# Kernel tuning notes

Measured on AMD Instinct MI355X. Metric: run time of the kernel, lower is better.

## Reference

```python
import jax, jax.numpy as jnp
import numpy as np

NUM_K_HEADS = 16
NUM_V_HEADS = 32
DK = 128
DV = 128
KCONV = 4
EPS = 1e-6
KEY_DIM = NUM_K_HEADS * DK      # 2048
VALUE_DIM = NUM_V_HEADS * DV    # 4096
HIDDEN = 2048
T_TOKENS = 4096


def setup_inputs() -> dict:
    key = jax.random.key(0)
    ks = jax.random.split(key, 10)
    s = 0.02
    return {
        "hidden_states": jax.random.normal(ks[0], (T_TOKENS, HIDDEN), jnp.float32),
        "W_qkv": jax.random.normal(ks[1], (2 * KEY_DIM + VALUE_DIM, HIDDEN), jnp.float32) * s,
        "W_z": jax.random.normal(ks[2], (VALUE_DIM, HIDDEN), jnp.float32) * s,
        "W_b": jax.random.normal(ks[3], (NUM_V_HEADS, HIDDEN), jnp.float32) * s,
        "W_a": jax.random.normal(ks[4], (NUM_V_HEADS, HIDDEN), jnp.float32) * s,
        "conv_weight": jax.random.normal(ks[5], (2 * KEY_DIM + VALUE_DIM, KCONV), jnp.float32) * 0.2,
        "dt_bias": jnp.ones((NUM_V_HEADS,), jnp.float32),
        "A_log": jax.random.normal(ks[6], (NUM_V_HEADS,), jnp.float32) * 0.5,
        "norm_weight": jnp.ones((DV,), jnp.float32),
        "W_out": jax.random.normal(ks[7], (HIDDEN, VALUE_DIM), jnp.float32) * s,
    }


def _l2norm(x):
    return x * jax.lax.rsqrt(jnp.sum(x * x, axis=-1, keepdims=True) + 1e-6)


def _gdn_forward(hidden_states, W_qkv, W_z, W_b, W_a, conv_weight,
                 dt_bias, A_log, norm_weight, W_out):
    T = hidden_states.shape[0]
    # input projections
    mixed_qkv = hidden_states @ W_qkv.T                         # [T, 2K+V]
    z = (hidden_states @ W_z.T).reshape(T, NUM_V_HEADS, DV)     # gate
    b = hidden_states @ W_b.T                                   # [T, Hv]
    a = hidden_states @ W_a.T                                   # [T, Hv]

    # depthwise causal conv1d (kernel 4) + silu, no bias
    xp = jnp.pad(mixed_qkv, ((KCONV - 1, 0), (0, 0)))
    conv = sum(xp[i:i + T] * conv_weight[:, i] for i in range(KCONV))
    x = jax.nn.silu(conv)

    q = x[:, :KEY_DIM].reshape(T, NUM_K_HEADS, DK)
    k = x[:, KEY_DIM:2 * KEY_DIM].reshape(T, NUM_K_HEADS, DK)
    v = x[:, 2 * KEY_DIM:].reshape(T, NUM_V_HEADS, DV)

    rep = NUM_V_HEADS // NUM_K_HEADS  # grouped value attention: repeat q/k heads
    q = jnp.repeat(_l2norm(q), rep, axis=1)  # [T, Hv, DK]
    k = jnp.repeat(_l2norm(k), rep, axis=1)

    beta = jax.nn.sigmoid(b)                                   # [T, Hv]
    g = -jnp.exp(A_log) * jax.nn.softplus(a + dt_bias)         # [T, Hv] log-decay
    scale = DK ** -0.5

    def step(S, inp):
        qt, kt, vt, bt, gt = inp
        S = S * jnp.exp(gt)[:, None, None]                     # gated decay
        kv = jnp.einsum('hk,hkv->hv', kt, S)                   # memory readout
        delta = (vt - kv) * bt[:, None]                        # delta rule update
        S = S + jnp.einsum('hk,hv->hkv', kt, delta)
        ot = jnp.einsum('hk,hkv->hv', qt, S) * scale
        return S, ot

    S0 = jnp.zeros((NUM_V_HEADS, DK, DV), mixed_qkv.dtype)
    _, o = jax.lax.scan(step, S0, (q, k, v, beta, g))          # o: [T, Hv, DV]

    # gated RMSNorm (norm before gate)
    var = jnp.mean(o * o, axis=-1, keepdims=True)
    on = o * jax.lax.rsqrt(var + EPS) * norm_weight
    y = on * jax.nn.silu(z)

    return y.reshape(T, VALUE_DIM) @ W_out.T                   # [T, HIDDEN]


def reference(hidden_states, W_qkv, W_z, W_b, W_a, conv_weight,
              dt_bias, A_log, norm_weight, W_out):
    return _gdn_forward(hidden_states, W_qkv, W_z, W_b, W_a, conv_weight,
                        dt_bias, A_log, norm_weight, W_out)
```

## Files before the change

### kernel.cpp

```cpp
#include <hip/hip_runtime.h>
#include <cstdint>
#include <cstddef>

typedef __bf16 bf16_t;
typedef __bf16 bf16x8 __attribute__((ext_vector_type(8)));
typedef __bf16 bf16x4 __attribute__((ext_vector_type(4)));
typedef float floatx4 __attribute__((ext_vector_type(4)));

__device__ __forceinline__ void async16(const bf16_t* g, bf16_t* l) {
  __builtin_amdgcn_global_load_lds(
      (const __attribute__((address_space(1))) unsigned int*)g,
      (__attribute__((address_space(3))) unsigned int*)l, 16, 0, 0);
}

__device__ __forceinline__ void barrier_lds() {
  asm volatile("s_waitcnt lgkmcnt(0)\n\ts_barrier" ::: "memory");
}

__device__ __forceinline__ float siluf(float x) { return x / (1.f + __expf(-x)); }

#define MFMA16(a, b, c) __builtin_amdgcn_mfma_f32_16x16x32_bf16(a, b, c, 0, 0, 0)
#define WAITV(n) asm volatile("s_waitcnt vmcnt(" #n ")" ::: "memory")

__global__ __launch_bounds__(256) void k_cvt(const float* __restrict__ in,
                                             bf16_t* __restrict__ out, int n4) {
  int i = blockIdx.x * 256 + threadIdx.x;
  if (i >= n4) return;
  const float4 f = ((const float4*)in)[i];
  bf16x4 r;
  r[0] = (bf16_t)f.x; r[1] = (bf16_t)f.y; r[2] = (bf16_t)f.z; r[3] = (bf16_t)f.w;
  ((bf16x4*)out)[i] = r;
}

__global__ __launch_bounds__(256) void k_build_wba(const float* __restrict__ wb,
                                                   const float* __restrict__ wa,
                                                   bf16_t* __restrict__ out) {
  int i = blockIdx.x * 256 + threadIdx.x;
  int e = i * 4;
  int row = e >> 11;
  int col = e & 2047;
  float4 f = make_float4(0.f, 0.f, 0.f, 0.f);
  if (row < 32)      f = *(const float4*)&wb[row * 2048 + col];
  else if (row < 64) f = *(const float4*)&wa[(row - 32) * 2048 + col];
  bf16x4 r;
  r[0] = (bf16_t)f.x; r[1] = (bf16_t)f.y; r[2] = (bf16_t)f.z; r[3] = (bf16_t)f.w;
  *(bf16x4*)&out[e] = r;
}

template<bool OUT_BF16>
__global__ __launch_bounds__(256) void gemm_bt(const bf16_t* __restrict__ A,
                                               const bf16_t* __restrict__ B,
                                               void* __restrict__ Cout,
                                               int M, int N, int K) {
  __shared__ __align__(16) bf16_t As[4096];
  __shared__ __align__(16) bf16_t Bs[4096];
  const int tid  = threadIdx.x;
  const int lane = tid & 63;
  const int wave = tid >> 6;
  const int quad = lane >> 4;
  const int l16  = lane & 15;
  const int wr   = (wave >> 1) * 64;
  const int wc   = (wave & 1) * 64;
  const int m0   = blockIdx.y * 128;
  const int n0   = blockIdx.x * 128;
  const int ra   = tid >> 2;
  const int ca   = (tid & 3) * 8;

  const bf16_t* gA = A + (size_t)(m0 + ra) * K + ca;
  const bf16_t* gB = B + (size_t)(n0 + ra) * K + ca;
  bf16_t* lA = &As[tid * 8];
  bf16_t* lB = &Bs[tid * 8];

  floatx4 acc[4][4] = {};

  for (int k0 = 0; k0 < K; k0 += 32) {
    __syncthreads();
    async16(gA + k0, lA);
    async16(gA + k0 + (size_t)64 * K, lA + 2048);
    async16(gB + k0, lB);
    async16(gB + k0 + (size_t)64 * K, lB + 2048);
    __syncthreads();
    bf16x8 af[4], bfr[4];
#pragma unroll
    for (int i = 0; i < 4; ++i) {
      af[i]  = *(const bf16x8*)&As[(wr + i * 16 + l16) * 32 + quad * 8];
      bfr[i] = *(const bf16x8*)&Bs[(wc + i * 16 + l16) * 32 + quad * 8];
    }
#pragma unroll
    for (int mi = 0; mi < 4; ++mi)
#pragma unroll
      for (int ni = 0; ni < 4; ++ni)
        acc[mi][ni] = MFMA16(af[mi], bfr[ni], acc[mi][ni]);
  }

#pragma unroll
  for (int mi = 0; mi < 4; ++mi) {
#pragma unroll
    for (int ni = 0; ni < 4; ++ni) {
      const int row = m0 + wr + mi * 16 + quad * 4;
      const int col = n0 + wc + ni * 16 + l16;
#pragma unroll
      for (int r = 0; r < 4; ++r) {
        if (OUT_BF16)
          ((bf16_t*)Cout)[(size_t)(row + r) * N + col] = (bf16_t)acc[mi][ni][r];
        else
          ((float*)Cout)[(size_t)(row + r) * N + col] = acc[mi][ni][r];
      }
    }
  }
}

template<int MH, bool OUT_BF16>
__global__ __launch_bounds__(512, 1) void gemm_big(const bf16_t* __restrict__ A,
                                                   const bf16_t* __restrict__ B,
                                                   void* __restrict__ Cout,
                                                   int M, int N, int K) {
  extern __shared__ __align__(16) bf16_t sm[];
  constexpr int BM    = MH * 128;
  constexpr int MFRAG = MH * 4;
  constexpr int HF    = MFRAG / 2;
  constexpr int BUFE  = MH * 4096 + 8192;
  const int tid  = threadIdx.x;
  const int lane = tid & 63;
  const int wave = tid >> 6;
  const int quad = lane >> 4;
  const int l16  = lane & 15;
  const int wm   = wave >> 2;
  const int wn   = wave & 3;

  const int gx  = (int)gridDim.x;
  const int nwg = gx * (int)gridDim.y;
  const int id  = (int)blockIdx.y * gx + (int)blockIdx.x;
  const int cpx = nwg >> 3;
  const int sw  = (id & 7) * cpx + (id >> 3);
  const int m0  = (sw / gx) * BM;
  const int n0  = (sw % gx) * 256;

  const int lr    = lane >> 2;
  const int lslot = (lane & 3) ^ ((lane >> 3) & 3);
  const bf16_t* gA = A + (size_t)(m0 + wave * (MH * 16) + lr) * K + lslot * 8;
  const bf16_t* gB = B + (size_t)(n0 + wave * 32 + lr) * K + lslot * 8;
  const int ldsA0 = wave * (MH * 512) + lane * 8;
  const int ldsB0 = MH * 4096 + wave * 1024 + lane * 8;

#define STG_A(u, kt) {                                          \
    bf16_t* la = sm + (u) * BUFE + ldsA0;                       \
    const bf16_t* ga = gA + (size_t)(kt) * 32;                  \
    async16(ga, la);                                            \
    if constexpr (MH == 2) async16(ga + (size_t)16 * K, la + 512); }
#define STG_B(u, kt) {                                          \
    bf16_t* lb = sm + (u) * BUFE + ldsB0;                       \
    const bf16_t* gb = gB + (size_t)(kt) * 32;                  \
    async16(gb, lb);                                            \
    async16(gb + (size_t)16 * K, lb + 512); }

  int offA[MFRAG], offB[4];
#pragma unroll
  for (int i = 0; i < MFRAG; ++i) {
    int ra = wm * (MFRAG * 16) + i * 16 + l16;
    offA[i] = (ra * 32 + quad * 8) ^ (((ra >> 1) & 3) << 3);
  }
#pragma unroll
  for (int i = 0; i < 4; ++i) {
    int rb = wn * 64 + i * 16 + l16;
    offB[i] = MH * 4096 + ((rb * 32 + quad * 8) ^ (((rb >> 1) & 3) << 3));
  }

  floatx4 acc[MFRAG][4] = {};
  const int KT = K >> 5;

  STG_A(0, 0); STG_B(0, 0);
  STG_A(1, 1); STG_B(1, 1);
  STG_A(2, 2); STG_B(2, 2);
  if constexpr (MH == 2) WAITV(8); else WAITV(6);
  asm volatile("s_barrier" ::: "memory");

  for (int U = 0; U < KT; ++U) {
    const int bu = U & 3;
    const bf16_t* sb = sm + bu * BUFE;
    const int un = U + 3;
    const int tu = un & 3;
    bf16x8 af[HF], bfr[4];

#pragma unroll
    for (int i = 0; i < HF; ++i) af[i] = *(const bf16x8*)&sb[offA[i]];
#pragma unroll
    for (int i = 0; i < 4; ++i) bfr[i] = *(const bf16x8*)&sb[offB[i]];
    if (un < KT) STG_A(tu, un);
    asm volatile("s_barrier" ::: "memory");
    __builtin_amdgcn_s_setprio(1);
#pragma unroll
    for (int mi = 0; mi < HF; ++mi)
#pragma unroll
      for (int ni = 0; ni < 4; ++ni)
        acc[mi][ni] = MFMA16(af[mi], bfr[ni], acc[mi][ni]);
    __builtin_amdgcn_s_setprio(0);
    asm volatile("s_barrier" ::: "memory");

#pragma unroll
    for (int i = 0; i < HF; ++i) af[i] = *(const bf16x8*)&sb[offA[HF + i]];
    if (un < KT) STG_B(tu, un);
    if (un < KT)         { if constexpr (MH == 2) WAITV(8); else WAITV(6); }
    else if (U + 2 < KT) { if constexpr (MH == 2) WAITV(4); else WAITV(3); }
    else                 WAITV(0);
    asm volatile("s_barrier" ::: "memory");
    __builtin_amdgcn_s_setprio(1);
#pragma unroll
    for (int mi = 0; mi < HF; ++mi)
#pragma unroll
      for (int ni = 0; ni < 4; ++ni)
        acc[HF + mi][ni] = MFMA16(af[mi], bfr[ni], acc[HF + mi][ni]);
    __builtin_amdgcn_s_setprio(0);
    asm volatile("s_barrier" ::: "memory");
  }
#undef STG_A
#undef STG_B

#pragma unroll
  for (int mi = 0; mi < MFRAG; ++mi) {
#pragma unroll
    for (int ni = 0; ni < 4; ++ni) {
      const int row = m0 + wm * (MFRAG * 16) + mi * 16 + quad * 4;
      const int col = n0 + wn * 64 + ni * 16 + l16;
#pragma unroll
      for (int r = 0; r < 4; ++r) {
        if (OUT_BF16)
          ((bf16_t*)Cout)[(size_t)(row + r) * N + col] = (bf16_t)acc[mi][ni][r];
        else
          ((float*)Cout)[(size_t)(row + r) * N + col] = acc[mi][ni][r];
      }
    }
  }
}

__global__ __launch_bounds__(256) void k_betag(const float* __restrict__ cba,
                                               const float* __restrict__ A_log,
                                               const float* __restrict__ dtb,
                                               float* __restrict__ beta_t,
                                               float* __restrict__ g_t) {
  int i = blockIdx.x * 256 + threadIdx.x;
  int t = i >> 5, h = i & 31;
  float b = cba[t * 128 + h];
  float a = cba[t * 128 + 32 + h];
  beta_t[h * 4096 + t] = 1.f / (1.f + __expf(-b));
  float x = a + dtb[h];
  float sp = (x > 20.f) ? x : log1pf(__expf(x));
  g_t[h * 4096 + t] = -__expf(A_log[h]) * sp;
}

__global__ __launch_bounds__(64) void k_conv(const bf16_t* __restrict__ mixed,
                                             const float* __restrict__ cw,
                                             bf16_t* __restrict__ qo,
                                             bf16_t* __restrict__ ko,
                                             bf16_t* __restrict__ vo) {
  const int grp = blockIdx.x;
  const int t0 = blockIdx.y * 8;
  const int l = threadIdx.x;
  const int c0 = grp * 128 + l;
  const int c1 = c0 + 64;
  const float4 w0 = *(const float4*)&cw[c0 * 4];
  const float4 w1 = *(const float4*)&cw[c1 * 4];
  float h0[3], h1[3];
#pragma unroll
  for (int j = 0; j < 3; ++j) {
    int tt = t0 - 3 + j;
    h0[j] = (tt >= 0) ? (float)mixed[(size_t)tt * 8192 + c0] : 0.f;
    h1[j] = (tt >= 0) ? (float)mixed[(size_t)tt * 8192 + c1] : 0.f;
  }
#pragma unroll
  for (int i = 0; i < 8; ++i) {
    const int t = t0 + i;
    float x0 = (float)mixed[(size_t)t * 8192 + c0];
    float x1 = (float)mixed[(size_t)t * 8192 + c1];
    float a0 = w0.x * h0[0] + w0.y * h0[1] + w0.z * h0[2] + w0.w * x0;
    float a1 = w1.x * h1[0] + w1.y * h1[1] + w1.z * h1[2] + w1.w * x1;
    h0[0] = h0[1]; h0[1] = h0[2]; h0[2] = x0;
    h1[0] = h1[1]; h1[1] = h1[2]; h1[2] = x1;
    float v0 = siluf(a0), v1 = siluf(a1);
    if (grp < 32) {
      float s = v0 * v0 + v1 * v1;
#pragma unroll
      for (int m = 1; m < 64; m <<= 1) s += __shfl_xor(s, m);
      float r = rsqrtf(s + 1e-6f);
      if (grp < 16) {
        bf16_t* q = qo + ((size_t)t * 16 + grp) * 128;
        q[l]      = (bf16_t)(v0 * r * 0.08838834764831845f);
        q[l + 64] = (bf16_t)(v1 * r * 0.08838834764831845f);
      } else {
        bf16_t* k = ko + ((size_t)t * 16 + grp - 16) * 128;
        k[l]      = (bf16_t)(v0 * r);
        k[l + 64] = (bf16_t)(v1 * r);
      }
    } else {
      bf16_t* v = vo + ((size_t)t * 32 + grp - 32) * 128;
      v[l]      = (bf16_t)v0;
      v[l + 64] = (bf16_t)v1;
    }
  }
}

__global__ __launch_bounds__(256, 2) void k_prep(
    const bf16_t* __restrict__ qg, const bf16_t* __restrict__ kg,
    const bf16_t* __restrict__ vg,
    const float* __restrict__ bb_t, const float* __restrict__ gb_t,
    bf16_t* __restrict__ Vt, bf16_t* __restrict__ Wlo, bf16_t* __restrict__ Whi,
    bf16_t* __restrict__ Mout, bf16_t* __restrict__ kt, float* __restrict__ smalls) {
  const int c = blockIdx.x >> 5;
  const int h = blockIdx.x & 31;
  const int kh = h >> 1;
  const int t0 = c * 64;
  const int tid = threadIdx.x, lane = tid & 63, wave = tid >> 6;
  const int quad = lane >> 4, l16 = lane & 15;

  __shared__ __align__(16) bf16_t lsKQ[2][64][136];
  __shared__ float lsC[64][68];
  __shared__ float lsG[64], lsA[64], lsSc[64], lsBeta[64];

  {
    const int r = tid >> 2, s0 = (tid & 3) * 32;
    const bf16_t* kr = kg + ((size_t)(t0 + r) * 16 + kh) * 128 + s0;
    const bf16_t* qr = qg + ((size_t)(t0 + r) * 16 + kh) * 128 + s0;
#pragma unroll
    for (int j = 0; j < 4; ++j) {
      *(uint4*)&lsKQ[0][r][s0 + j * 8] = *(const uint4*)&kr[j * 8];
      *(uint4*)&lsKQ[1][r][s0 + j * 8] = *(const uint4*)&qr[j * 8];
    }
  }
  if (wave == 0) {
    float gv = gb_t[(size_t)h * 4096 + t0 + lane];
#pragma unroll
    for (int off = 1; off < 64; off <<= 1) {
      float n = __shfl_up(gv, off);
      if (lane >= off) gv += n;
    }
    float GL = __shfl(gv, 63);
    lsG[lane] = gv;
    lsA[lane] = __expf(gv);
    lsSc[lane] = __expf(GL - gv);
    lsBeta[lane] = bb_t[(size_t)h * 4096 + t0 + lane];
  }
  __syncthreads();

  const int mr = (wave >> 1) * 32, nr = (wave & 1) * 32;
  floatx4 ak[2][2] = {}, aq[2][2] = {};
  if (wave != 1) {
#pragma unroll
    for (int ks = 0; ks < 4; ++ks) {
      bf16x8 yf[2], xk[2], xq[2];
#pragma unroll
      for (int i = 0; i < 2; ++i) {
        yf[i] = *(const bf16x8*)&lsKQ[0][nr + i * 16 + l16][ks * 32 + quad * 8];
        xk[i] = *(const bf16x8*)&lsKQ[0][mr + i * 16 + l16][ks * 32 + quad * 8];
        xq[i] = *(const bf16x8*)&lsKQ[1][mr + i * 16 + l16][ks * 32 + quad * 8];
      }
#pragma unroll
      for (int i = 0; i < 2; ++i)
#pragma unroll
        for (int j = 0; j < 2; ++j) {
          ak[i][j] = MFMA16(xk[i], yf[j], ak[i][j]);
          aq[i][j] = MFMA16(xq[i], yf[j], aq[i][j]);
        }
    }
  }
  bf16_t* Mb = Mout + (size_t)(h * 64 + c) * 4096;
#pragma unroll
  for (int i = 0; i < 2; ++i)
#pragma unroll
    for (int j = 0; j < 2; ++j)
#pragma unroll
      for (int r = 0; r < 4; ++r) {
        int t = mr + i * 16 + quad * 4 + r;
        int s = nr + j * 16 + l16;
        float e = __expf(lsG[t] - lsG[s]);
        float cv = (s < t) ? lsBeta[t] * e * ak[i][j][r] : 0.f;
        float mv = (s <= t) ? e * aq[i][j][r] : 0.f;
        if (wave != 1) lsC[t][s] = cv;
        Mb[t * 64 + s] = (bf16_t)mv;
      }
  __syncthreads();

  const int col = tid & 127;
  const bool isW = tid >= 128;
  float vals[64];
#pragma unroll
  for (int t = 0; t < 64; ++t) {
    float b;
    if (!isW) b = (float)vg[((size_t)(t0 + t) * 32 + h) * 128 + col];
    else      b = lsA[t] * (float)lsKQ[0][t][col];
    vals[t] = lsBeta[t] * b;
  }
#pragma unroll
  for (int t = 1; t < 64; ++t) {
    float acc = vals[t];
#pragma unroll
    for (int s4 = 0; s4 <= (t - 1) >> 2; ++s4) {
      float4 cv = *(const float4*)&lsC[t][s4 * 4];
      acc -= cv.x * vals[s4 * 4 + 0];
      acc -= cv.y * vals[s4 * 4 + 1];
      acc -= cv.z * vals[s4 * 4 + 2];
      acc -= cv.w * vals[s4 * 4 + 3];
    }
    vals[t] = acc;
  }

  if (!isW) {
    bf16_t* vd = Vt + (size_t)(h * 64 + c) * 8192 + (size_t)col * 64;
#pragma unroll
    for (int j = 0; j < 16; ++j) {
      bf16x4 p;
      p[0] = (bf16_t)vals[j * 4 + 0];
      p[1] = (bf16_t)vals[j * 4 + 1];
      p[2] = (bf16_t)vals[j * 4 + 2];
      p[3] = (bf16_t)vals[j * 4 + 3];
      *(bf16x4*)&vd[j * 4] = p;
    }
  } else {
#pragma unroll
    for (int t = 0; t < 64; ++t) vals[t] = -vals[t];
  }

  if ((h & 1) == 0) {
    const int dk = tid >> 1, sh = (tid & 1) * 32;
    bf16_t* kd = kt + (size_t)(c * 16 + kh) * 8192 + (size_t)dk * 64 + sh;
#pragma unroll
    for (int j4 = 0; j4 < 4; ++j4) {
      bf16x8 v;
#pragma unroll
      for (int e = 0; e < 8; ++e) v[e] = lsKQ[0][sh + j4 * 8 + e][dk];
      *(bf16x8*)&kd[j4 * 8] = v;
    }
  }
  if (tid < 64) {
    float* sm = smalls + (size_t)(h * 64 + c) * 128;
    sm[tid] = lsA[tid];
    sm[64 + tid] = lsSc[tid];
  }
  __syncthreads();

  bf16_t* lsT = &lsKQ[0][0][0];
  if (isW) {
#pragma unroll
    for (int t = 0; t < 64; ++t) lsT[t * 272 + tid] = (bf16_t)vals[t];
  }
  __syncthreads();

  {
    const int r = tid >> 2, part = tid & 3;
    const bf16_t* src = &lsT[r * 272 + 128 + part * 32];
    bf16_t* Wb = (h < 16 ? Wlo : Whi) + (size_t)((h & 15) * 64 + c) * 8192 + r * 128 + part * 32;
#pragma unroll
    for (int j = 0; j < 4; ++j)
      *(uint4*)&Wb[j * 8] = *(const uint4*)&src[j * 8];
  }
}

__global__ __launch_bounds__(256, 1) void k_chain(
    const bf16_t* __restrict__ qg, const bf16_t* __restrict__ VtT,
    const bf16_t* __restrict__ Wlo, const bf16_t* __restrict__ Whi,
    const bf16_t* __restrict__ Mg, const bf16_t* __restrict__ ktg,
    const float* __restrict__ smalls, bf16_t* __restrict__ o) {
  const int h = blockIdx.x & 31;
  const int dv0 = (blockIdx.x >> 5) * 16;
  const int kh = h >> 1;
  const int tid = threadIdx.x, lane = tid & 63, wave = tid >> 6;
  const int quad = lane >> 4, l16 = lane & 15;
  const int trow = wave * 16 + quad * 4;

  __shared__ __align__(16) bf16_t lsXT[16][72];
  __shared__ __align__(16) bf16_t lsXbT[16][72];
  __shared__ __align__(16) bf16_t lsS[16][136];

  const bf16_t* Wbase = (h < 16 ? Wlo : Whi) + (size_t)(h & 15) * 64 * 8192;
  const bf16_t* Vbase = VtT + (size_t)h * 64 * 8192;
  const bf16_t* Mbase = Mg + (size_t)h * 64 * 4096;
  const float*  Sbase = smalls + (size_t)h * 64 * 128;

  const bf16_t* pW = Wbase + (size_t)(wave * 16 + l16) * 128 + quad * 8;
  const bf16_t* pQ = qg + ((size_t)(wave * 16 + l16) * 16 + kh) * 128 + quad * 8;
  const bf16_t* pK = ktg + (size_t)kh * 8192 + (size_t)(wave * 16 + l16) * 64 + quad * 8;
  const bf16_t* pM = Mbase + (size_t)(wave * 16 + l16) * 64 + quad * 8;
  const bf16_t* pV = Vbase + (size_t)(dv0 + l16) * 64 + trow;
  const float*  pS = Sbase;

  floatx4 sacc[2] = {};
  for (int i = tid; i < 16 * 136; i += 256) (&lsS[0][0])[i] = (bf16_t)0.f;

  bf16x8 nW[4], nQ[4], nK[4], nM[2];
  bf16x4 nV;
  float4 nA, nSc;
  float nAL;
  {
#pragma unroll
    for (int ks = 0; ks < 4; ++ks) {
      nW[ks] = *(const bf16x8*)&pW[ks * 32];
      nQ[ks] = *(const bf16x8*)&pQ[ks * 32];
    }
    nK[0] = *(const bf16x8*)&pK[0];
    nK[1] = *(const bf16x8*)&pK[32];
    nK[2] = *(const bf16x8*)&pK[4096];
    nK[3] = *(const bf16x8*)&pK[4096 + 32];
    nM[0] = *(const bf16x8*)&pM[0];
    nM[1] = *(const bf16x8*)&pM[32];
    nV = *(const bf16x4*)&pV[0];
    nA  = *(const float4*)&pS[trow];
    nSc = *(const float4*)&pS[64 + trow];
    nAL = pS[63];
    pW += 8192; pQ += 131072; pK += 131072; pM += 4096; pV += 8192; pS += 128;
  }
  __syncthreads();

  for (int cc = 0; cc < 64; ++cc) {
    const int t0 = cc * 64;
    bf16x8 cW[4], cQ[4], cK[4], cM[2];
    float cV[4];
    float4 cA = nA, cSc = nSc;
    float cAL = nAL;
#pragma unroll
    for (int ks = 0; ks < 4; ++ks) { cW[ks] = nW[ks]; cQ[ks] = nQ[ks]; cK[ks] = nK[ks]; }
    cM[0] = nM[0]; cM[1] = nM[1];
#pragma unroll
    for (int r = 0; r < 4; ++r) cV[r] = (float)nV[r];

    if (cc + 1 < 64) {
#pragma unroll
      for (int ks = 0; ks < 4; ++ks) {
        nW[ks] = *(const bf16x8*)&pW[ks * 32];
        nQ[ks] = *(const bf16x8*)&pQ[ks * 32];
      }
      nK[0] = *(const bf16x8*)&pK[0];
      nK[1] = *(const bf16x8*)&pK[32];
      nK[2] = *(const bf16x8*)&pK[4096];
      nK[3] = *(const bf16x8*)&pK[4096 + 32];
      nM[0] = *(const bf16x8*)&pM[0];
      nM[1] = *(const bf16x8*)&pM[32];
      nV = *(const bf16x4*)&pV[0];
      nA  = *(const float4*)&pS[trow];
      nSc = *(const float4*)&pS[64 + trow];
      nAL = pS[63];
      pW += 8192; pQ += 131072; pK += 131072; pM += 4096; pV += 8192; pS += 128;
    }

    bf16x8 bS[4];
#pragma unroll
    for (int ks = 0; ks < 4; ++ks)
      bS[ks] = *(const bf16x8*)&lsS[l16][ks * 32 + quad * 8];
    floatx4 xacc;
#pragma unroll
    for (int r = 0; r < 4; ++r) xacc[r] = cV[r];
#pragma unroll
    for (int ks = 0; ks < 4; ++ks)
      xacc = MFMA16(cW[ks], bS[ks], xacc);
    {
      bf16x4 px, pb;
#pragma unroll
      for (int r = 0; r < 4; ++r) {
        px[r] = (bf16_t)xacc[r];
        pb[r] = (bf16_t)(xacc[r] * ((const float*)&cSc)[r]);
      }
      *(bf16x4*)&lsXT[l16][trow] = px;
      *(bf16x4*)&lsXbT[l16][trow] = pb;
    }
    floatx4 qacc = {};
#pragma unroll
    for (int ks = 0; ks < 4; ++ks)
      qacc = MFMA16(cQ[ks], bS[ks], qacc);
#pragma unroll
    for (int r = 0; r < 4; ++r) qacc[r] *= ((const float*)&cA)[r];
#pragma unroll
    for (int mh = 0; mh < 2; ++mh)
#pragma unroll
      for (int r = 0; r < 4; ++r) sacc[mh][r] *= cAL;
    barrier_lds();

#pragma unroll
    for (int ks = 0; ks < 2; ++ks) {
      bf16x8 bX = *(const bf16x8*)&lsXT[l16][ks * 32 + quad * 8];
      qacc = MFMA16(cM[ks], bX, qacc);
    }
#pragma unroll
    for (int r = 0; r < 4; ++r)
      o[((size_t)(t0 + trow + r) * 32 + h) * 128 + dv0 + l16] = (bf16_t)qacc[r];

#pragma unroll
    for (int ks = 0; ks < 2; ++ks) {
      bf16x8 bXb = *(const bf16x8*)&lsXbT[l16][ks * 32 + quad * 8];
#pragma unroll
      for (int mh = 0; mh < 2; ++mh)
        sacc[mh] = MFMA16(cK[mh * 2 + ks], bXb, sacc[mh]);
    }
#pragma unroll
    for (int mh = 0; mh < 2; ++mh) {
      bf16x4 ps;
#pragma unroll
      for (int r = 0; r < 4; ++r) ps[r] = (bf16_t)sacc[mh][r];
      *(bf16x4*)&lsS[l16][(wave + 4 * mh) * 16 + quad * 4] = ps;
    }
    barrier_lds();
  }
}

__global__ __launch_bounds__(256) void k_gate(const bf16_t* __restrict__ o,
                                              const bf16_t* __restrict__ z,
                                              const float* __restrict__ nw,
                                              bf16_t* __restrict__ y) {
  const int row = blockIdx.x * 4 + (threadIdx.x >> 6);
  const int l = threadIdx.x & 63;
  const bf16_t* orow = o + (size_t)row * 128;
  float o0 = (float)orow[l], o1 = (float)orow[l + 64];
  float s = o0 * o0 + o1 * o1;
#pragma unroll
  for (int m = 1; m < 64; m <<= 1) s += __shfl_xor(s, m);
  float r = rsqrtf(s * (1.f / 128.f) + 1e-6f);
  const bf16_t* zrow = z + (size_t)row * 128;
  float z0 = (float)zrow[l], z1 = (float)zrow[l + 64];
  bf16_t* yrow = y + (size_t)row * 128;
  yrow[l]      = (bf16_t)(o0 * r * nw[l] * siluf(z0));
  yrow[l + 64] = (bf16_t)(o1 * r * nw[l + 64] * siluf(z1));
}

extern "C" void kernel_launch(void* const* d_in, const int* in_sizes, int n_in,
                              void* d_out, int out_size, void* d_ws, size_t ws_size,
                              hipStream_t stream) {
  const float* hidden = (const float*)d_in[0];
  const float* W_qkv  = (const float*)d_in[1];
  const float* W_z    = (const float*)d_in[2];
  const float* W_b    = (const float*)d_in[3];
  const float* W_a    = (const float*)d_in[4];
  const float* conv_w = (const float*)d_in[5];
  const float* dt_b   = (const float*)d_in[6];
  const float* A_log  = (const float*)d_in[7];
  const float* norm_w = (const float*)d_in[8];
  const float* W_out  = (const float*)d_in[9];
  float* out = (float*)d_out;

  static int gemm_attr_done = 0;
  if (!gemm_attr_done) {
    hipFuncSetAttribute(reinterpret_cast<const void*>(&gemm_big<2, true>),
                        hipFuncAttributeMaxDynamicSharedMemorySize, 131072);
    hipFuncSetAttribute(reinterpret_cast<const void*>(&gemm_big<1, false>),
                        hipFuncAttributeMaxDynamicSharedMemorySize, 98304);
    gemm_attr_done = 1;
  }

  char* w = (char*)d_ws;
  const size_t MB = 1024 * 1024;
  bf16_t* hs    = (bf16_t*)(w + 0 * MB);
  bf16_t* Wlo   = hs;
  bf16_t* wqkv  = (bf16_t*)(w + 16 * MB);
  bf16_t* Vtb   = wqkv;
  bf16_t* ybuf  = wqkv;
  bf16_t* wz    = (bf16_t*)(w + 48 * MB);
  bf16_t* Whi   = wz;
  bf16_t* wout  = (bf16_t*)(w + 64 * MB);
  bf16_t* wba   = (bf16_t*)(w + 80 * MB);
  bf16_t* mixed = (bf16_t*)(w + 81 * MB);
  bf16_t* obuf  = mixed;
  bf16_t* Mbuf  = (bf16_t*)(w + 113 * MB);
  bf16_t* ktb   = (bf16_t*)(w + 129 * MB);
  bf16_t* zbuf  = (bf16_t*)(w + 145 * MB);
  float*  cba   = (float*)(w + 177 * MB);
  float*  smalls= cba;
  bf16_t* qb    = (bf16_t*)(w + 179 * MB);
  bf16_t* kb    = (bf16_t*)(w + 195 * MB);
  bf16_t* vb    = (bf16_t*)(w + 211 * MB);
  float*  betab = (float*)(w + 243 * MB);
  float*  gbuf  = (float*)(w + 243 * MB + 512 * 1024);

  k_cvt<<<8192, 256, 0, stream>>>(hidden, hs, 2097152);
  k_cvt<<<16384, 256, 0, stream>>>(W_qkv, wqkv, 4194304);
  k_cvt<<<8192, 256, 0, stream>>>(W_z, wz, 2097152);
  k_cvt<<<8192, 256, 0, stream>>>(W_out, wout, 2097152);
  k_build_wba<<<256, 256, 0, stream>>>(W_b, W_a, wba);

  gemm_big<2, true><<<dim3(32, 16), 512, 131072, stream>>>(hs, wqkv, mixed, 4096, 8192, 2048);
  gemm_big<2, true><<<dim3(16, 16), 512, 131072, stream>>>(hs, wz, zbuf, 4096, 4096, 2048);
  gemm_bt<false><<<dim3(1, 32), 256, 0, stream>>>(hs, wba, cba, 4096, 128, 2048);
  k_betag<<<512, 256, 0, stream>>>(cba, A_log, dt_b, betab, gbuf);

  k_conv<<<dim3(64, 512), 64, 0, stream>>>(mixed, conv_w, qb, kb, vb);

  k_prep<<<2048, 256, 0, stream>>>(qb, kb, vb, betab, gbuf,
                                   Vtb, Wlo, Whi, Mbuf, ktb, smalls);
  k_chain<<<256, 256, 0, stream>>>(qb, Vtb, Wlo, Whi, Mbuf, ktb, smalls, obuf);

  k_gate<<<32768, 256, 0, stream>>>(obuf, zbuf, norm_w, ybuf);
  gemm_big<1, false><<<dim3(8, 32), 512, 98304, stream>>>(ybuf, wout, out, 4096, 2048, 4096);
}
```

Baseline: 829.1 us.

## Add 256x256 K64 double-buffered GEMM with XCD-aware tile swizzle for input projections

Adds a new GEMM kernel for the QKV and Z projections. It uses a 256x256 output tile with K-step 64, double-buffered LDS split into half-tile stages, and a four-phase schedule of LDS reads and MFMAs interleaved with async global-to-LDS loads. Workgroup IDs are remapped in groups of eight so that neighbouring tiles land on the same XCD, which should improve L2 reuse. It replaces the previous four-stage K32 pipeline for these two GEMMs, giving fewer barriers per FLOP at the cost of a tighter double-buffer prefetch distance.

Result: no change. 816.7 us (-1.5%).

```diff
diff --git a/kernel.cpp b/kernel.cpp
--- a/kernel.cpp
+++ b/kernel.cpp
@@ -21,6 +21,7 @@
 
 #define MFMA16(a, b, c) __builtin_amdgcn_mfma_f32_16x16x32_bf16(a, b, c, 0, 0, 0)
 #define WAITV(n) asm volatile("s_waitcnt vmcnt(" #n ")" ::: "memory")
+#define SBAR() asm volatile("s_barrier" ::: "memory")
 
 __global__ __launch_bounds__(256) void k_cvt(const float* __restrict__ in,
                                              bf16_t* __restrict__ out, int n4) {
@@ -110,6 +111,156 @@
   }
 }
 
+template<bool OUT_BF16>
+__global__ __launch_bounds__(512, 1) void gemm8p(const bf16_t* __restrict__ A,
+                                                 const bf16_t* __restrict__ B,
+                                                 void* __restrict__ Cout,
+                                                 int M, int N, int K) {
+  extern __shared__ __align__(16) bf16_t sm[];
+  const int tid  = threadIdx.x;
+  const int lane = tid & 63;
+  const int wave = tid >> 6;
+  const int quad = lane >> 4;
+  const int l16  = lane & 15;
+  const int wm   = wave >> 2;
+  const int wn   = wave & 3;
+
+  const int gx  = (int)gridDim.x;
+  const int nwg = gx * (int)gridDim.y;
+  const int id  = (int)blockIdx.y * gx + (int)blockIdx.x;
+  const int cpx = nwg >> 3;
+  const int sw  = (id & 7) * cpx + (id >> 3);
+  const int m0  = (sw / gx) * 256;
+  const int n0  = (sw % gx) * 256;
+
+  const int rowg   = tid >> 3;
+  const int colsrc = (tid & 7) ^ (rowg & 7);
+  const bf16_t* gAs = A + (size_t)(m0 + rowg) * K + colsrc * 8;
+  const bf16_t* gBs = B + (size_t)(n0 + rowg) * K + colsrc * 8;
+  bf16_t* lds0 = sm + tid * 8;
+
+#define STG_A8(u, kt, ht) {                                     \
+    bf16_t* la = lds0 + (u) * 32768 + (ht) * 8192;              \
+    const bf16_t* ga = gAs + (size_t)(ht) * 128 * K + (kt) * 64;\
+    async16(ga, la); async16(ga + (size_t)64 * K, la + 4096); }
+#define STG_B8(u, kt, ht) {                                     \
+    bf16_t* lb = lds0 + (u) * 32768 + 16384 + (ht) * 8192;      \
+    const bf16_t* gb = gBs + (size_t)(ht) * 128 * K + (kt) * 64;\
+    async16(gb, lb); async16(gb + (size_t)64 * K, lb + 4096); }
+
+  const int x7  = l16 & 7;
+  const int cA0 = ((quad + 0) ^ x7) * 8;
+  const int cA1 = ((quad + 4) ^ x7) * 8;
+  const int eA0 = (wm * 128 + l16) * 64;
+  const int eB0 = 16384 + (wn * 64 + l16) * 64;
+
+  floatx4 acc[8][4] = {};
+  const int KT = K >> 6;
+
+  STG_A8(0, 0, 0); STG_A8(0, 0, 1);
+  STG_B8(0, 0, 0); STG_B8(0, 0, 1);
+  STG_B8(1, 1, 0); STG_B8(1, 1, 1);
+  WAITV(4);
+  SBAR();
+
+  bf16x8 af[4][2], bn0[2][2], bn1[2][2];
+  for (int X = 0; X < KT; ++X) {
+    const int c = X & 1;
+    const bf16_t* sb = sm + c * 32768;
+
+#pragma unroll
+    for (int i = 0; i < 4; ++i) {
+      af[i][0] = *(const bf16x8*)&sb[eA0 + i * 1024 + cA0];
+      af[i][1] = *(const bf16x8*)&sb[eA0 + i * 1024 + cA1];
+    }
+#pragma unroll
+    for (int j = 0; j < 2; ++j) {
+      bn0[j][0] = *(const bf16x8*)&sb[eB0 + j * 1024 + cA0];
+      bn0[j][1] = *(const bf16x8*)&sb[eB0 + j * 1024 + cA1];
+    }
+    if (X + 1 < KT) STG_A8(c ^ 1, X + 1, 0);
+    SBAR();
+    __builtin_amdgcn_s_setprio(1);
+#pragma unroll
+    for (int i = 0; i < 4; ++i)
+#pragma unroll
+      for (int j = 0; j < 2; ++j) {
+        acc[i][j] = MFMA16(af[i][0], bn0[j][0], acc[i][j]);
+        acc[i][j] = MFMA16(af[i][1], bn0[j][1], acc[i][j]);
+      }
+    __builtin_amdgcn_s_setprio(0);
+    SBAR();
+
+#pragma unroll
+    for (int j = 0; j < 2; ++j) {
+      bn1[j][0] = *(const bf16x8*)&sb[eB0 + (2 + j) * 1024 + cA0];
+      bn1[j][1] = *(const bf16x8*)&sb[eB0 + (2 + j) * 1024 + cA1];
+    }
+    if (X + 1 < KT) STG_A8(c ^ 1, X + 1, 1);
+    SBAR();
+    __builtin_amdgcn_s_setprio(1);
+#pragma unroll
+    for (int i = 0; i < 4; ++i)
+#pragma unroll
+      for (int j = 0; j < 2; ++j) {
+        acc[i][2 + j] = MFMA16(af[i][0], bn1[j][0], acc[i][2 + j]);
+        acc[i][2 + j] = MFMA16(af[i][1], bn1[j][1], acc[i][2 + j]);
+      }
+    __builtin_amdgcn_s_setprio(0);
+    SBAR();
+
+#pragma unroll
+    for (int i = 0; i < 4; ++i) {
+      af[i][0] = *(const bf16x8*)&sb[eA0 + (4 + i) * 1024 + cA0];
+      af[i][1] = *(const bf16x8*)&sb[eA0 + (4 + i) * 1024 + cA1];
+    }
+    if (X + 2 < KT) STG_B8(c, X + 2, 0);
+    SBAR();
+    __builtin_amdgcn_s_setprio(1);
+#pragma unroll
+    for (int i = 0; i < 4; ++i)
+#pragma unroll
+      for (int j = 0; j < 2; ++j) {
+        acc[4 + i][j] = MFMA16(af[i][0], bn0[j][0], acc[4 + i][j]);
+        acc[4 + i][j] = MFMA16(af[i][1], bn0[j][1], acc[4 + i][j]);
+      }
+    __builtin_amdgcn_s_setprio(0);
+    SBAR();
+
+    if (X + 2 < KT) { STG_B8(c, X + 2, 1); WAITV(4); }
+    else            { WAITV(0); }
+    SBAR();
+    __builtin_amdgcn_s_setprio(1);
+#pragma unroll
+    for (int i = 0; i < 4; ++i)
+#pragma unroll
+      for (int j = 0; j < 2; ++j) {
+        acc[4 + i][2 + j] = MFMA16(af[i][0], bn1[j][0], acc[4 + i][2 + j]);
+        acc[4 + i][2 + j] = MFMA16(af[i][1], bn1[j][1], acc[4 + i][2 + j]);
+      }
+    __builtin_amdgcn_s_setprio(0);
+    SBAR();
+  }
+#undef STG_A8
+#undef STG_B8
+
+#pragma unroll
+  for (int mi = 0; mi < 8; ++mi) {
+#pragma unroll
+    for (int ni = 0; ni < 4; ++ni) {
+      const int row = m0 + wm * 128 + mi * 16 + quad * 4;
+      const int col = n0 + wn * 64 + ni * 16 + l16;
+#pragma unroll
+      for (int r = 0; r < 4; ++r) {
+        if (OUT_BF16)
+          ((bf16_t*)Cout)[(size_t)(row + r) * N + col] = (bf16_t)acc[mi][ni][r];
+        else
+          ((float*)Cout)[(size_t)(row + r) * N + col] = acc[mi][ni][r];
+      }
+    }
+  }
+}
+
 template<int MH, bool OUT_BF16>
 __global__ __launch_bounds__(512, 1) void gemm_big(const bf16_t* __restrict__ A,
                                                    const bf16_t* __restrict__ B,
@@ -173,7 +324,7 @@
   STG_A(1, 1); STG_B(1, 1);
   STG_A(2, 2); STG_B(2, 2);
   if constexpr (MH == 2) WAITV(8); else WAITV(6);
-  asm volatile("s_barrier" ::: "memory");
+  SBAR();
 
   for (int U = 0; U < KT; ++U) {
     const int bu = U & 3;
@@ -187,7 +338,7 @@
 #pragma unroll
     for (int i = 0; i < 4; ++i) bfr[i] = *(const bf16x8*)&sb[offB[i]];
     if (un < KT) STG_A(tu, un);
-    asm volatile("s_barrier" ::: "memory");
+    SBAR();
     __builtin_amdgcn_s_setprio(1);
 #pragma unroll
     for (int mi = 0; mi < HF; ++mi)
@@ -195,7 +346,7 @@
       for (int ni = 0; ni < 4; ++ni)
         acc[mi][ni] = MFMA16(af[mi], bfr[ni], acc[mi][ni]);
     __builtin_amdgcn_s_setprio(0);
-    asm volatile("s_barrier" ::: "memory");
+    SBAR();
 
 #pragma unroll
     for (int i = 0; i < HF; ++i) af[i] = *(const bf16x8*)&sb[offA[HF + i]];
@@ -203,7 +354,7 @@
     if (un < KT)         { if constexpr (MH == 2) WAITV(8); else WAITV(6); }
     else if (U + 2 < KT) { if constexpr (MH == 2) WAITV(4); else WAITV(3); }
     else                 WAITV(0);
-    asm volatile("s_barrier" ::: "memory");
+    SBAR();
     __builtin_amdgcn_s_setprio(1);
 #pragma unroll
     for (int mi = 0; mi < HF; ++mi)
@@ -211,7 +362,7 @@
       for (int ni = 0; ni < 4; ++ni)
         acc[HF + mi][ni] = MFMA16(af[mi], bfr[ni], acc[HF + mi][ni]);
     __builtin_amdgcn_s_setprio(0);
-    asm volatile("s_barrier" ::: "memory");
+    SBAR();
   }
 #undef STG_A
 #undef STG_B
@@ -635,7 +786,7 @@
 
   static int gemm_attr_done = 0;
   if (!gemm_attr_done) {
-    hipFuncSetAttribute(reinterpret_cast<const void*>(&gemm_big<2, true>),
+    hipFuncSetAttribute(reinterpret_cast<const void*>(&gemm8p<true>),
                         hipFuncAttributeMaxDynamicSharedMemorySize, 131072);
     hipFuncSetAttribute(reinterpret_cast<const void*>(&gemm_big<1, false>),
                         hipFuncAttributeMaxDynamicSharedMemorySize, 98304);
@@ -672,8 +823,8 @@
   k_cvt<<<8192, 256, 0, stream>>>(W_out, wout, 2097152);
   k_build_wba<<<256, 256, 0, stream>>>(W_b, W_a, wba);
 
-  gemm_big<2, true><<<dim3(32, 16), 512, 131072, stream>>>(hs, wqkv, mixed, 4096, 8192, 2048);
-  gemm_big<2, true><<<dim3(16, 16), 512, 131072, stream>>>(hs, wz, zbuf, 4096, 4096, 2048);
+  gemm8p<true><<<dim3(32, 16), 512, 131072, stream>>>(hs, wqkv, mixed, 4096, 8192, 2048);
+  gemm8p<true><<<dim3(16, 16), 512, 131072, stream>>>(hs, wz, zbuf, 4096, 4096, 2048);
   gemm_bt<false><<<dim3(1, 32), 256, 0, stream>>>(hs, wba, cba, 4096, 128, 2048);
   k_betag<<<512, 256, 0, stream>>>(cba, A_log, dt_b, betab, gbuf);
 
```
